# Kernel tuning notes

Hardware: AMD Instinct MI355X
Metric: run time of the kernel (lower is better)

Reference implementation:

```python
import jax, jax.numpy as jnp
import numpy as np

N = 50000      # nodes
E = 1200000    # edges
G = 256        # graphs in batch
H = 64         # hidden_dim
F_IN = 5       # input_dim
L = 3          # num deep GCN layers
EPS_BN = 1e-5
EPS_MSG = 1e-7

def setup_inputs() -> dict:
    key = jax.random.key(0)
    ks = jax.random.split(key, 12)
    r = lambda i, shp, s=0.1: jax.random.normal(ks[i], shp, jnp.float32) * s
    return {
        "x": jax.random.normal(ks[0], (N, F_IN), jnp.float32),
        "edge_index": jax.random.randint(ks[1], (2, E), 0, N),
        "batch_idx": jnp.sort(jax.random.randint(ks[2], (N,), 0, G)),
        "conv1_W": r(3, (F_IN, H)), "conv1_b": jnp.zeros((H,), jnp.float32),
        "bn1_g": jnp.ones((H,), jnp.float32), "bn1_b": jnp.zeros((H,), jnp.float32),
        "ln_g": jnp.ones((L, H), jnp.float32), "ln_b": jnp.zeros((L, H), jnp.float32),
        "prelu_a": jnp.full((L, H), 0.25, jnp.float32),
        "gen_t": jnp.ones((L,), jnp.float32),
        "mlp_W1": r(4, (L, H, 2 * H)), "mlp_b1": jnp.zeros((L, 2 * H), jnp.float32),
        "mlp_bn_g": jnp.ones((L, 2 * H), jnp.float32), "mlp_bn_b": jnp.zeros((L, 2 * H), jnp.float32),
        "mlp_W2": r(5, (L, 2 * H, H)), "mlp_b2": jnp.zeros((L, H), jnp.float32),
        "lin1_W": r(6, ((L + 1) * H * 2, 2 * H)), "lin1_b": jnp.zeros((2 * H,), jnp.float32),
        "lin2_W": r(7, (2 * H, H)), "lin2_b": jnp.zeros((H,), jnp.float32),
        "out_W": r(8, (H, 1)), "out_b": jnp.zeros((1,), jnp.float32),
    }

def _layernorm(x, g, b):
    mu = jnp.mean(x, axis=-1, keepdims=True)
    var = jnp.mean(jnp.square(x - mu), axis=-1, keepdims=True)
    return (x - mu) * jax.lax.rsqrt(var + EPS_BN) * g + b

def _prelu(x, a):
    return jnp.where(x >= 0, x, a * x)

def _bn_eval(x, g, b):
    # eval-mode BatchNorm with running_mean=0, running_var=1
    return x * (g / jnp.sqrt(1.0 + EPS_BN)) + b

def reference(x, edge_index, batch_idx, conv1_W, conv1_b, bn1_g, bn1_b,
              ln_g, ln_b, prelu_a, gen_t, mlp_W1, mlp_b1, mlp_bn_g, mlp_bn_b,
              mlp_W2, mlp_b2, lin1_W, lin1_b, lin2_W, lin2_b, out_W, out_b):
    n = x.shape[0]
    src, dst = edge_index[0], edge_index[1]

    # ---- GCNConv (with self loops, symmetric normalization) ----
    loops = jnp.arange(n)
    row = jnp.concatenate([src, loops])  # [E+N]
    col = jnp.concatenate([dst, loops])
    h = x @ conv1_W
    deg = jax.ops.segment_sum(jnp.ones_like(col, jnp.float32), col, num_segments=n)
    dinv = jnp.where(deg > 0, deg ** -0.5, 0.0)
    norm = dinv[row] * dinv[col]
    h = jax.ops.segment_sum(h[row] * norm[:, None], col, num_segments=n) + conv1_b
    h = _bn_eval(h, bn1_g, bn1_b)
    h = jax.nn.relu(h)

    xs = [h]
    # ---- DeepGCNLayer (res+) x L, GENConv with softmax aggregation ----
    for i in range(ln_g.shape[0]):
        u = _layernorm(h, ln_g[i], ln_b[i])
        u = _prelu(u, prelu_a[i])
        msg = jax.nn.relu(u[src]) + EPS_MSG            # [E, H]
        sc = msg * gen_t[i]
        m = jax.ops.segment_max(sc, dst, num_segments=n)
        e = jnp.exp(sc - m[dst])
        s = jax.ops.segment_sum(e, dst, num_segments=n)
        alpha = e / s[dst]                             # segment-wise softmax per channel
        agg = jax.ops.segment_sum(msg * alpha, dst, num_segments=n) + u  # root add
        z = agg @ mlp_W1[i] + mlp_b1[i]
        z = _bn_eval(z, mlp_bn_g[i], mlp_bn_b[i])
        z = jax.nn.relu(z)
        z = z @ mlp_W2[i] + mlp_b2[i]
        h = h + z                                      # res+
        xs.append(h)

    # ---- JumpingKnowledge cat + global mean/max pool ----
    xc = jnp.concatenate(xs, axis=1)                   # [N, 4H]
    cnt = jax.ops.segment_sum(jnp.ones((n,), jnp.float32), batch_idx, num_segments=G)
    xmean = jax.ops.segment_sum(xc, batch_idx, num_segments=G) / jnp.maximum(cnt, 1.0)[:, None]
    xmax = jax.ops.segment_max(xc, batch_idx, num_segments=G)
    xmax = jnp.where(jnp.isfinite(xmax), xmax, 0.0)
    p = jnp.concatenate([xmean, xmax], axis=1)         # [G, 8H]

    # ---- readout MLP (dropout off in eval) ----
    p = jax.nn.relu(p @ lin1_W + lin1_b)
    p = jax.nn.relu(p @ lin2_W + lin2_b)
    return p @ out_W + out_b
```

## Files before the change

kernel.cpp:

```cpp
#include <hip/hip_runtime.h>
#include <math.h>

#define NND 50000
#define NE  1200000
#define NG  256
#define H   64
#define H2  128
#define H4  256
#define H8  512
#define FIN 5
#define EPS_BN 1e-5f
#define EPS_MSG 1e-7f
#define NB 196
#define TILES 196
#define TCAP 7168
#define EPB 4096
#define NB1 293
#define MRG (NB + 14)
#define ELLC 72
#define MT 64

typedef _Float16 half8 __attribute__((ext_vector_type(8)));
typedef _Float16 half4 __attribute__((ext_vector_type(4)));
typedef float floatx4 __attribute__((ext_vector_type(4)));

__device__ __forceinline__ unsigned fmap_max(float f) {
    unsigned b = __float_as_uint(f);
    return (b & 0x80000000u) ? ~b : (b | 0x80000000u);
}


__global__ void __launch_bounds__(256)
k_setup(const int* __restrict__ batch, int* tilecur, int* __restrict__ gstart,
        const float* __restrict__ x, float* __restrict__ xp,
        const float* __restrict__ W1, const float* __restrict__ W2,
        _Float16* __restrict__ w1f, _Float16* __restrict__ w2f,
        const int* __restrict__ ei, unsigned* __restrict__ tilebuf) {
    __shared__ int cnt[TILES];
    __shared__ int base[TILES];
    int b = blockIdx.x, t = threadIdx.x;
    if (b >= MRG) {
        int bb = b - MRG;
        for (int i = t; i < TILES; i += 256) cnt[i] = 0;
        __syncthreads();
        int e0 = bb * EPB;
#pragma unroll
        for (int r = 0; r < EPB / 256; r++) {
            int e = e0 + r * 256 + t;
            if (e < NE) atomicAdd(&cnt[ei[NE + e] >> 8], 1);
        }
        __syncthreads();
        for (int i = t; i < TILES; i += 256) {
            base[i] = atomicAdd(&tilecur[i], cnt[i]);
            cnt[i] = 0;
        }
        __syncthreads();
#pragma unroll
        for (int r = 0; r < EPB / 256; r++) {
            int e = e0 + r * 256 + t;
            if (e < NE) {
                int s = ei[e], d = ei[NE + e];
                int tile = d >> 8;
                int pos = base[tile] + atomicAdd(&cnt[tile], 1);
                if (pos < TCAP)
                    tilebuf[(size_t)tile * TCAP + pos] = ((unsigned)s << 8) | (unsigned)(d & 255);
            }
        }
        return;
    }
    if (b < NB) {
        int n = b * 256 + t;
        if (n < NND) {
            float a0 = x[n * FIN + 0], a1 = x[n * FIN + 1], a2 = x[n * FIN + 2];
            float a3 = x[n * FIN + 3], a4 = x[n * FIN + 4];
            *(float4*)&xp[n * 8] = make_float4(a0, a1, a2, a3);
            *(float4*)&xp[n * 8 + 4] = make_float4(a4, 0.f, 0.f, 0.f);
        }
        return;
    }
    if (b == NB || b == NB + 1) {
        int g = (b - NB) * 256 + t;
        if (g > NG) return;
        int lo = 0, hi = NND;
        while (lo < hi) { int mid = (lo + hi) >> 1; if (batch[mid] < g) lo = mid + 1; else hi = mid; }
        gstart[g] = lo;
        return;
    }
    int tt = (b - NB - 2) * 256 + t;
    if (tt >= 3 * 16 * 64) return;
    int lane = tt & 63, fr = (tt >> 6) & 15, l = tt >> 10;
    {
        int jt = fr >> 1, kf = fr & 1;
        int j = jt * 16 + (lane & 15);
        int k0 = kf * 32 + (lane >> 4) * 8;
#pragma unroll
        for (int i = 0; i < 8; i++)
            w1f[(((size_t)l * 16 + jt * 2 + kf) * 64 + lane) * 8 + i] =
                (_Float16)W1[(size_t)l * H * H2 + (k0 + i) * H2 + j];
    }
    {
        int ct = fr >> 2, k2f = fr & 3;
        int c = ct * 16 + (lane & 15);
        int k0 = k2f * 32 + (lane >> 4) * 8;
#pragma unroll
        for (int i = 0; i < 8; i++)
            w2f[(((size_t)l * 16 + ct * 4 + k2f) * 64 + lane) * 8 + i] =
                (_Float16)W2[(size_t)l * H2 * H + (k0 + i) * H + c];
    }
}


__global__ void __launch_bounds__(256)
k_bin2(const int* __restrict__ tilecur, const unsigned* __restrict__ tilebuf,
       unsigned short* __restrict__ ell, int* __restrict__ deg, float* __restrict__ xp) {
    __shared__ unsigned short ell_l[256 * ELLC];
    __shared__ int cnt[256];
    int tile = blockIdx.x, t = threadIdx.x;
    cnt[t] = 0;
    __syncthreads();
    int n = min(tilecur[tile], TCAP);
    for (int i = t; i < n; i += 256) {
        unsigned v = __builtin_nontemporal_load(&tilebuf[(size_t)tile * TCAP + i]);
        int dl = v & 255u;
        int slot = atomicAdd(&cnt[dl], 1);
        if (slot < ELLC) ell_l[dl * ELLC + slot] = (unsigned short)(v >> 8);
    }
    __syncthreads();
    const unsigned* s32 = (const unsigned*)ell_l;
    unsigned* d32 = (unsigned*)(ell + (size_t)tile * 256 * ELLC);
    for (int i = t; i < 256 * ELLC / 2; i += 256) d32[i] = s32[i];
    int d = tile * 256 + t;
    if (d < NND) {
        deg[d] = min(cnt[t], ELLC);
        xp[(size_t)d * 8 + 5] = rsqrtf((float)cnt[t] + 1.0f);
    }
}


__global__ void k_gcn(const int* __restrict__ deg, const unsigned short* __restrict__ ell,
                      const float* __restrict__ xp,
                      const float* __restrict__ W,
                      const float* __restrict__ cb, const float* __restrict__ bg,
                      const float* __restrict__ bb,
                      const float* __restrict__ lg, const float* __restrict__ lb,
                      const float* __restrict__ pa,
                      _Float16* __restrict__ xcH, _Float16* __restrict__ u_h,
                      const int* __restrict__ batch,
                      float* __restrict__ psum, unsigned* __restrict__ pmax_u) {
    __shared__ float ps[4][64];
    __shared__ float pm[4][64];
    int tid = blockIdx.x * blockDim.x + threadIdx.x;
    int d = tid >> 4;
    int r = threadIdx.x & 15;
    if (d >= NND) return;
    int dg = deg[d];
    size_t base = (size_t)d * ELLC;
    float xw0 = 0.f, xw1 = 0.f, xw2 = 0.f, xw3 = 0.f, xw4 = 0.f;
    for (int i = r; i < dg; i += 16) {
        int s = (int)__builtin_nontemporal_load(&ell[base + i]);
        float4 a = *(const float4*)&xp[s * 8];
        float2 a45 = *(const float2*)&xp[s * 8 + 4];
        float dv = a45.y;
        xw0 += a.x * dv; xw1 += a.y * dv; xw2 += a.z * dv;
        xw3 += a.w * dv; xw4 += a45.x * dv;
    }
#pragma unroll
    for (int off = 1; off <= 8; off <<= 1) {
        xw0 += __shfl_xor(xw0, off, 64);
        xw1 += __shfl_xor(xw1, off, 64);
        xw2 += __shfl_xor(xw2, off, 64);
        xw3 += __shfl_xor(xw3, off, 64);
        xw4 += __shfl_xor(xw4, off, 64);
    }
    float4 xa = *(const float4*)&xp[d * 8];
    float2 xa45 = *(const float2*)&xp[d * 8 + 4];
    float dd = xa45.y;
    xw0 += dd * xa.x; xw1 += dd * xa.y; xw2 += dd * xa.z;
    xw3 += dd * xa.w; xw4 += dd * xa45.x;
    float bns = rsqrtf(1.f + EPS_BN);
    float x0[4];
    float sum = 0.f, sq = 0.f;
#pragma unroll
    for (int j = 0; j < 4; j++) {
        int c = 4 * r + j;
        float s_ = xw0 * W[c] + xw1 * W[H + c] + xw2 * W[2 * H + c]
                 + xw3 * W[3 * H + c] + xw4 * W[4 * H + c];
        float v = s_ * dd + cb[c];
        v = v * (bg[c] * bns) + bb[c];
        v = fmaxf(v, 0.f);
        x0[j] = v;
        sum += v; sq += v * v;
    }
    {
        half4 xh = {(_Float16)x0[0], (_Float16)x0[1], (_Float16)x0[2], (_Float16)x0[3]};
        *(half4*)&xcH[(size_t)d * H4 + 4 * r] = xh;
    }
#pragma unroll
    for (int off = 1; off <= 8; off <<= 1) {
        sum += __shfl_xor(sum, off, 64);
        sq  += __shfl_xor(sq,  off, 64);
    }
    float mu  = sum * (1.f / H);
    float var = sq * (1.f / H) - mu * mu;
    float rs = rsqrtf(var + EPS_BN);
    half4 yh;
#pragma unroll
    for (int j = 0; j < 4; j++) {
        int c = 4 * r + j;
        float y = (x0[j] - mu) * rs * lg[c] + lb[c];
        y = (y >= 0.f) ? y : pa[c] * y;
        yh[j] = (_Float16)y;
    }
    *(half4*)&u_h[(size_t)d * H + 4 * r] = yh;

    int first = blockIdx.x * 16;
    int gd = batch[d];
    int g_lo = batch[first], g_hi = batch[first + 15];
    int w = threadIdx.x >> 6;
    for (int g = g_lo; g <= g_hi; ++g) {
        bool m_ = (gd == g);
        float s0 = m_ ? x0[0] : 0.f, s1 = m_ ? x0[1] : 0.f;
        float s2 = m_ ? x0[2] : 0.f, s3 = m_ ? x0[3] : 0.f;
        float m0 = m_ ? x0[0] : -INFINITY, m1 = m_ ? x0[1] : -INFINITY;
        float m2 = m_ ? x0[2] : -INFINITY, m3 = m_ ? x0[3] : -INFINITY;
#pragma unroll
        for (int off = 16; off <= 32; off <<= 1) {
            s0 += __shfl_xor(s0, off, 64); s1 += __shfl_xor(s1, off, 64);
            s2 += __shfl_xor(s2, off, 64); s3 += __shfl_xor(s3, off, 64);
            m0 = fmaxf(m0, __shfl_xor(m0, off, 64)); m1 = fmaxf(m1, __shfl_xor(m1, off, 64));
            m2 = fmaxf(m2, __shfl_xor(m2, off, 64)); m3 = fmaxf(m3, __shfl_xor(m3, off, 64));
        }
        if ((threadIdx.x & 63) < 16) {
            ps[w][4 * r + 0] = s0; ps[w][4 * r + 1] = s1;
            ps[w][4 * r + 2] = s2; ps[w][4 * r + 3] = s3;
            pm[w][4 * r + 0] = m0; pm[w][4 * r + 1] = m1;
            pm[w][4 * r + 2] = m2; pm[w][4 * r + 3] = m3;
        }
        __syncthreads();
        if (threadIdx.x < 64) {
            float S = (ps[0][threadIdx.x] + ps[1][threadIdx.x]) +
                      (ps[2][threadIdx.x] + ps[3][threadIdx.x]);
            float M = fmaxf(fmaxf(pm[0][threadIdx.x], pm[1][threadIdx.x]),
                            fmaxf(pm[2][threadIdx.x], pm[3][threadIdx.x]));
            atomicAdd(&psum[(size_t)g * H4 + threadIdx.x], S);
            atomicMax(&pmax_u[(size_t)g * H4 + threadIdx.x], fmap_max(M));
        }
        __syncthreads();
    }
}


__global__ void k_gen(const int* __restrict__ deg, const unsigned short* __restrict__ ell,
                      const _Float16* __restrict__ u_h,
                      const float* __restrict__ tptr, int li, _Float16* __restrict__ ua_h) {
    int d = (blockIdx.x * blockDim.x + threadIdx.x) >> 6;
    int lane = threadIdx.x & 63;
    if (d >= NND) return;
    int q = lane & 15, eg = lane >> 4;
    float t = tptr[li];
    int dg = deg[d];
    size_t base = (size_t)d * ELLC;
    half4 us = *(const half4*)&u_h[(size_t)d * H + 4 * q];
    float4 s4 = {0.f, 0.f, 0.f, 0.f}, n4 = {0.f, 0.f, 0.f, 0.f};
    for (int i0 = 0; i0 < dg; i0 += 64) {
        int idx = i0 + lane;
        int csrv = (idx < dg) ? (int)__builtin_nontemporal_load(&ell[base + idx]) : 0;
        int chunk = min(64, dg - i0);
        for (int j = 0; j < chunk; j += 32) {
            half4 uv[8]; bool ok[8];
#pragma unroll
            for (int b2 = 0; b2 < 8; b2++) {
                int e_rel = j + 4 * b2 + eg;
                int s = __shfl(csrv, e_rel, 64);
                ok[b2] = (e_rel < chunk);
                uv[b2] = (half4){0, 0, 0, 0};
                if (ok[b2]) uv[b2] = *(const half4*)&u_h[(size_t)s * H + 4 * q];
            }
#pragma unroll
            for (int b2 = 0; b2 < 8; b2++) {
                if (ok[b2]) {
                    float m0 = fmaxf((float)uv[b2][0], 0.f) + EPS_MSG;
                    float m1 = fmaxf((float)uv[b2][1], 0.f) + EPS_MSG;
                    float m2 = fmaxf((float)uv[b2][2], 0.f) + EPS_MSG;
                    float m3 = fmaxf((float)uv[b2][3], 0.f) + EPS_MSG;
                    float e0 = __expf(m0 * t - 8.f);
                    float e1 = __expf(m1 * t - 8.f);
                    float e2 = __expf(m2 * t - 8.f);
                    float e3 = __expf(m3 * t - 8.f);
                    s4.x += e0; s4.y += e1; s4.z += e2; s4.w += e3;
                    n4.x += m0 * e0; n4.y += m1 * e1; n4.z += m2 * e2; n4.w += m3 * e3;
                }
            }
        }
    }
#pragma unroll
    for (int off = 16; off <= 32; off <<= 1) {
        s4.x += __shfl_xor(s4.x, off, 64); s4.y += __shfl_xor(s4.y, off, 64);
        s4.z += __shfl_xor(s4.z, off, 64); s4.w += __shfl_xor(s4.w, off, 64);
        n4.x += __shfl_xor(n4.x, off, 64); n4.y += __shfl_xor(n4.y, off, 64);
        n4.z += __shfl_xor(n4.z, off, 64); n4.w += __shfl_xor(n4.w, off, 64);
    }
    if (eg == 0) {
        float o0 = (float)us[0] + ((s4.x > 0.f) ? n4.x / s4.x : 0.f);
        float o1 = (float)us[1] + ((s4.y > 0.f) ? n4.y / s4.y : 0.f);
        float o2 = (float)us[2] + ((s4.z > 0.f) ? n4.z / s4.z : 0.f);
        float o3 = (float)us[3] + ((s4.w > 0.f) ? n4.w / s4.w : 0.f);
        half4 oh = {(_Float16)o0, (_Float16)o1, (_Float16)o2, (_Float16)o3};
        *(half4*)&ua_h[(size_t)d * H + 4 * q] = oh;
    }
}


__global__ void __launch_bounds__(256)
k_mlp(const _Float16* __restrict__ ua_h,
      const _Float16* __restrict__ w1f, const _Float16* __restrict__ w2f,
      const float* __restrict__ b1,
      const float* __restrict__ bng, const float* __restrict__ bnb,
      const float* __restrict__ b2,
      _Float16* __restrict__ xcH, int slice,
      const float* __restrict__ lg, const float* __restrict__ lb,
      const float* __restrict__ pa, _Float16* __restrict__ u_h, int do_ln,
      const int* __restrict__ batch,
      float* __restrict__ psum, unsigned* __restrict__ pmax_u) {
    __shared__ _Float16 a2[4][4][64][8];
    __shared__ float pls[4][64];
    __shared__ float plm[4][64];
    int t = threadIdx.x;
    int w = t >> 6, l = t & 63;
    int nb = blockIdx.x * MT;
    int c_in = l & 15, quad = l >> 4;
    bool wvalid = (nb + 16 * w) < NND;

    half8 af0 = {0,0,0,0,0,0,0,0}, af1 = af0;
    {
        int node = nb + 16 * w + c_in;
        if (node < NND) {
            af0 = *(const half8*)&ua_h[(size_t)node * H + quad * 8];
            af1 = *(const half8*)&ua_h[(size_t)node * H + 32 + quad * 8];
        }
    }

    floatx4 acc[8];
#pragma unroll
    for (int jt = 0; jt < 8; jt++) acc[jt] = (floatx4){0.f, 0.f, 0.f, 0.f};
#pragma unroll
    for (int jt = 0; jt < 8; jt++) {
        half8 bf0 = *(const half8*)&w1f[((size_t)(jt * 2 + 0) * 64 + l) * 8];
        half8 bf1 = *(const half8*)&w1f[((size_t)(jt * 2 + 1) * 64 + l) * 8];
        acc[jt] = __builtin_amdgcn_mfma_f32_16x16x32_f16(af0, bf0, acc[jt], 0, 0, 0);
        acc[jt] = __builtin_amdgcn_mfma_f32_16x16x32_f16(af1, bf1, acc[jt], 0, 0, 0);
    }

    {
        float bns = rsqrtf(1.f + EPS_BN);
#pragma unroll
        for (int jt = 0; jt < 8; jt++) {
            int j = jt * 16 + c_in;
            float b1v = b1[j], bsv = bng[j] * bns, bbv = bnb[j];
            int kf2 = jt >> 1;
            int lp = 16 * ((2 * jt + (c_in >> 3)) & 3);
            int ii = c_in & 7;
#pragma unroll
            for (int reg = 0; reg < 4; reg++) {
                float z = fmaxf((acc[jt][reg] + b1v) * bsv + bbv, 0.f);
                a2[w][kf2][quad * 4 + reg + lp][ii] = (_Float16)z;
            }
        }
    }

    floatx4 acc2[4];
#pragma unroll
    for (int ct = 0; ct < 4; ct++) acc2[ct] = (floatx4){0.f, 0.f, 0.f, 0.f};
    half8 a2f[4];
#pragma unroll
    for (int k2f = 0; k2f < 4; k2f++) a2f[k2f] = *(half8*)&a2[w][k2f][l][0];
#pragma unroll
    for (int ct = 0; ct < 4; ct++) {
#pragma unroll
        for (int k2f = 0; k2f < 4; k2f++) {
            half8 bfr = *(const half8*)&w2f[((size_t)(ct * 4 + k2f) * 64 + l) * 8];
            acc2[ct] = __builtin_amdgcn_mfma_f32_16x16x32_f16(a2f[k2f], bfr, acc2[ct], 0, 0, 0);
        }
    }

    float vv[4][4];
#pragma unroll
    for (int ct = 0; ct < 4; ct++) {
        int c = ct * 16 + c_in;
        float b2v = b2[c];
#pragma unroll
        for (int reg = 0; reg < 4; reg++) {
            int node = nb + 16 * w + quad * 4 + reg;
            float v = 0.f;
            if (wvalid) {
                v = (float)xcH[(size_t)node * H4 + slice * H + c] + acc2[ct][reg] + b2v;
                xcH[(size_t)node * H4 + (slice + 1) * H + c] = (_Float16)v;
            }
            vv[ct][reg] = v;
        }
    }
    if (do_ln) {
#pragma unroll
        for (int reg = 0; reg < 4; reg++) {
            float s = (vv[0][reg] + vv[1][reg]) + (vv[2][reg] + vv[3][reg]);
            float q = (vv[0][reg] * vv[0][reg] + vv[1][reg] * vv[1][reg]) +
                      (vv[2][reg] * vv[2][reg] + vv[3][reg] * vv[3][reg]);
#pragma unroll
            for (int off = 1; off <= 8; off <<= 1) {
                s += __shfl_xor(s, off, 64);
                q += __shfl_xor(q, off, 64);
            }
            float mu = s * (1.f / H);
            float var = q * (1.f / H) - mu * mu;
            float rs = rsqrtf(var + EPS_BN);
            int node = nb + 16 * w + quad * 4 + reg;
#pragma unroll
            for (int ct = 0; ct < 4; ct++) {
                int c = ct * 16 + c_in;
                float y = (vv[ct][reg] - mu) * rs * lg[c] + lb[c];
                y = (y >= 0.f) ? y : pa[c] * y;
                if (wvalid) u_h[(size_t)node * H + c] = (_Float16)y;
            }
        }
    }

    int gd_r[4];
#pragma unroll
    for (int reg = 0; reg < 4; reg++) {
        int node = nb + 16 * w + quad * 4 + reg;
        gd_r[reg] = (node < NND) ? batch[node] : -1;
    }
    int g_lo = batch[nb];
    int g_hi = batch[min(nb + 63, NND - 1)];
    int chbase = (slice + 1) * H;
    for (int g = g_lo; g <= g_hi; ++g) {
        float sc[4], mc[4];
#pragma unroll
        for (int ct = 0; ct < 4; ct++) {
            float s_ = 0.f, m_ = -INFINITY;
#pragma unroll
            for (int reg = 0; reg < 4; reg++) {
                if (gd_r[reg] == g) { s_ += vv[ct][reg]; m_ = fmaxf(m_, vv[ct][reg]); }
            }
            sc[ct] = s_; mc[ct] = m_;
        }
#pragma unroll
        for (int off = 16; off <= 32; off <<= 1) {
#pragma unroll
            for (int ct = 0; ct < 4; ct++) {
                sc[ct] += __shfl_xor(sc[ct], off, 64);
                mc[ct] = fmaxf(mc[ct], __shfl_xor(mc[ct], off, 64));
            }
        }
        if (l < 16) {
#pragma unroll
            for (int ct = 0; ct < 4; ct++) {
                pls[w][ct * 16 + l] = sc[ct];
                plm[w][ct * 16 + l] = mc[ct];
            }
        }
        __syncthreads();
        if (t < 64) {
            float S = (pls[0][t] + pls[1][t]) + (pls[2][t] + pls[3][t]);
            float M = fmaxf(fmaxf(plm[0][t], plm[1][t]), fmaxf(plm[2][t], plm[3][t]));
            atomicAdd(&psum[(size_t)g * H4 + chbase + t], S);
            atomicMax(&pmax_u[(size_t)g * H4 + chbase + t], fmap_max(M));
        }
        __syncthreads();
    }
}


__global__ void __launch_bounds__(256)
k_readout(const float* __restrict__ psum, const unsigned* __restrict__ pmax_u,
          const int* __restrict__ gstart,
          const float* __restrict__ W1, const float* __restrict__ b1,
          const float* __restrict__ W2, const float* __restrict__ b2,
          const float* __restrict__ Wo, const float* __restrict__ bo,
          float* __restrict__ out) {
    __shared__ float p0_l[H8];
    __shared__ float p1part[2][H2];
    __shared__ float p1_l[H2];
    __shared__ float p2part[4][H];
    __shared__ float p2_l[H];
    int g = blockIdx.x;
    int t = threadIdx.x;

    {
        int cnt = gstart[g + 1] - gstart[g];
        float s = psum[(size_t)g * H4 + t];
        unsigned u = pmax_u[(size_t)g * H4 + t];
        float m = (u & 0x80000000u) ? __uint_as_float(u & 0x7FFFFFFFu) : __uint_as_float(~u);
        p0_l[t] = s / fmaxf((float)cnt, 1.f);
        p0_l[H4 + t] = (cnt > 0) ? m : 0.f;
    }
    __syncthreads();

    {
        int j = t & 127, h = t >> 7;
        float acc = 0.f;
        int k0 = h * 256;
        for (int k = 0; k < 256; k++) acc += p0_l[k0 + k] * W1[(k0 + k) * H2 + j];
        p1part[h][j] = acc;
    }
    __syncthreads();
    if (t < H2) p1_l[t] = fmaxf(p1part[0][t] + p1part[1][t] + b1[t], 0.f);
    __syncthreads();

    {
        int c = t & 63, h = t >> 6;
        float acc = 0.f;
        int k0 = h * 32;
        for (int k = 0; k < 32; k++) acc += p1_l[k0 + k] * W2[(k0 + k) * H + c];
        p2part[h][c] = acc;
    }
    __syncthreads();
    if (t < H) p2_l[t] = fmaxf(((p2part[0][t] + p2part[1][t]) + (p2part[2][t] + p2part[3][t])) + b2[t], 0.f);
    __syncthreads();

    if (t < 64) {
        float v = p2_l[t] * Wo[t];
#pragma unroll
        for (int off = 32; off >= 1; off >>= 1) v += __shfl_xor(v, off, 64);
        if (t == 0) out[g] = v + bo[0];
    }
}

extern "C" void kernel_launch(void* const* d_in, const int* in_sizes, int n_in,
                              void* d_out, int out_size, void* d_ws, size_t ws_size,
                              hipStream_t stream) {
    const float* x       = (const float*)d_in[0];
    const int*   ei      = (const int*)d_in[1];
    const int*   batch   = (const int*)d_in[2];
    const float* conv1_W = (const float*)d_in[3];
    const float* conv1_b = (const float*)d_in[4];
    const float* bn1_g   = (const float*)d_in[5];
    const float* bn1_b   = (const float*)d_in[6];
    const float* ln_g    = (const float*)d_in[7];
    const float* ln_b    = (const float*)d_in[8];
    const float* prelu_a = (const float*)d_in[9];
    const float* gen_t   = (const float*)d_in[10];
    const float* mlp_W1  = (const float*)d_in[11];
    const float* mlp_b1  = (const float*)d_in[12];
    const float* mlp_bng = (const float*)d_in[13];
    const float* mlp_bnb = (const float*)d_in[14];
    const float* mlp_W2  = (const float*)d_in[15];
    const float* mlp_b2  = (const float*)d_in[16];
    const float* lin1_W  = (const float*)d_in[17];
    const float* lin1_b  = (const float*)d_in[18];
    const float* lin2_W  = (const float*)d_in[19];
    const float* lin2_b  = (const float*)d_in[20];
    const float* out_W   = (const float*)d_in[21];
    const float* out_b   = (const float*)d_in[22];
    float* out = (float*)d_out;

    float* ws   = (float*)d_ws;
    _Float16* xcH = (_Float16*)ws;
    float* xp   = (float*)(xcH + (size_t)NND * H4);
    int* deg    = (int*)(xp + (size_t)NND * 8);
    int* gstart = deg + NND;
    int* tilecur = gstart + NG + 1;
    unsigned* tilebuf = (unsigned*)(tilecur + TILES);
    unsigned short* ell = (unsigned short*)(tilebuf + (size_t)TILES * TCAP);
    uintptr_t wb = (uintptr_t)(ell + (size_t)TILES * 256 * ELLC);
    wb = (wb + 15) & ~(uintptr_t)15;
    _Float16* w1f = (_Float16*)wb;
    _Float16* w2f = w1f + 3 * 8192;
    _Float16* u_h  = w2f + 3 * 8192;
    _Float16* ua_h = u_h + (size_t)NND * H;
    uintptr_t pb = (uintptr_t)(ua_h + (size_t)NND * H);
    pb = (pb + 15) & ~(uintptr_t)15;
    float* psum = (float*)pb;
    unsigned* pmax_u = (unsigned*)(psum + (size_t)NG * H4);

    const int B = 256;
    const int gGCN = (NND * 16 + B - 1) / B;
    const int gNH  = (NND * H) / B;
    const int gMLP = (NND + MT - 1) / MT;

    hipMemsetAsync(tilecur, 0, TILES * sizeof(int), stream);
    hipMemsetAsync(psum, 0, (size_t)NG * H4 * (sizeof(float) + sizeof(unsigned)), stream);
    k_setup<<<MRG + NB1, B, 0, stream>>>(batch, tilecur, gstart, x, xp,
                                         mlp_W1, mlp_W2, w1f, w2f, ei, tilebuf);
    k_bin2<<<TILES, B, 0, stream>>>(tilecur, tilebuf, ell, deg, xp);

    k_gcn<<<gGCN, B, 0, stream>>>(deg, ell, xp, conv1_W, conv1_b, bn1_g, bn1_b,
                                  ln_g, ln_b, prelu_a, xcH, u_h,
                                  batch, psum, pmax_u);

    for (int i = 0; i < 3; i++) {
        k_gen<<<gNH, B, 0, stream>>>(deg, ell, u_h, gen_t, i, ua_h);
        int do_ln = (i < 2) ? 1 : 0;
        k_mlp<<<gMLP, B, 0, stream>>>(ua_h,
                                      w1f + (size_t)i * 8192, w2f + (size_t)i * 8192,
                                      mlp_b1 + i * H2,
                                      mlp_bng + i * H2, mlp_bnb + i * H2,
                                      mlp_b2 + i * H,
                                      xcH, i,
                                      ln_g + (i + 1) * H, ln_b + (i + 1) * H,
                                      prelu_a + (i + 1) * H, u_h, do_ln,
                                      batch, psum, pmax_u);
    }

    k_readout<<<NG, B, 0, stream>>>(psum, pmax_u, gstart,
                                    lin1_W, lin1_b, lin2_W, lin2_b, out_W, out_b, out);
}
```

Before: 332.8 us.

## Precompute per-node softmax exp terms in producer kernels instead of per edge

The GENConv softmax numerator and weighted message terms (exp(m*t) and m*exp(m*t)) are now computed once per source node in k_gcn and k_mlp and stored as interleaved fp16 in a new buffer. k_gen then only gathers and sums these precomputed pairs per edge instead of evaluating exp for every edge. This removes per-edge transcendental work but doubles the bytes gathered per edge and adds fp16 rounding and overflow risk on the exp values.

```diff
diff --git a/kernel.cpp b/kernel.cpp
--- a/kernel.cpp
+++ b/kernel.cpp
@@ -22,6 +22,7 @@
 
 typedef _Float16 half8 __attribute__((ext_vector_type(8)));
 typedef _Float16 half4 __attribute__((ext_vector_type(4)));
+typedef _Float16 half2 __attribute__((ext_vector_type(2)));
 typedef float floatx4 __attribute__((ext_vector_type(4)));
 
 __device__ __forceinline__ unsigned fmap_max(float f) {
@@ -146,7 +147,8 @@
                       const float* __restrict__ pa,
                       _Float16* __restrict__ xcH, _Float16* __restrict__ u_h,
                       const int* __restrict__ batch,
-                      float* __restrict__ psum, unsigned* __restrict__ pmax_u) {
+                      float* __restrict__ psum, unsigned* __restrict__ pmax_u,
+                      const float* __restrict__ gent, _Float16* __restrict__ emf) {
     __shared__ float ps[4][64];
     __shared__ float pm[4][64];
     int tid = blockIdx.x * blockDim.x + threadIdx.x;
@@ -203,15 +205,22 @@
     float mu  = sum * (1.f / H);
     float var = sq * (1.f / H) - mu * mu;
     float rs = rsqrtf(var + EPS_BN);
+    float t0 = gent[0];
     half4 yh;
+    half8 emh;
 #pragma unroll
     for (int j = 0; j < 4; j++) {
         int c = 4 * r + j;
         float y = (x0[j] - mu) * rs * lg[c] + lb[c];
         y = (y >= 0.f) ? y : pa[c] * y;
         yh[j] = (_Float16)y;
+        float m_ = fmaxf(y, 0.f) + EPS_MSG;
+        float ex = __expf(m_ * t0 - 8.f);
+        emh[2 * j]     = (_Float16)ex;
+        emh[2 * j + 1] = (_Float16)(m_ * ex);
     }
     *(half4*)&u_h[(size_t)d * H + 4 * r] = yh;
+    *(half8*)&emf[(size_t)d * 128 + 8 * r] = emh;
 
     int first = blockIdx.x * 16;
     int gd = batch[d];
@@ -251,13 +260,12 @@
 
 
 __global__ void k_gen(const int* __restrict__ deg, const unsigned short* __restrict__ ell,
-                      const _Float16* __restrict__ u_h,
-                      const float* __restrict__ tptr, int li, _Float16* __restrict__ ua_h) {
+                      const _Float16* __restrict__ u_h, const _Float16* __restrict__ emf,
+                      _Float16* __restrict__ ua_h) {
     int d = (blockIdx.x * blockDim.x + threadIdx.x) >> 6;
     int lane = threadIdx.x & 63;
     if (d >= NND) return;
     int q = lane & 15, eg = lane >> 4;
-    float t = tptr[li];
     int dg = deg[d];
     size_t base = (size_t)d * ELLC;
     half4 us = *(const half4*)&u_h[(size_t)d * H + 4 * q];
@@ -267,29 +275,20 @@
         int csrv = (idx < dg) ? (int)__builtin_nontemporal_load(&ell[base + idx]) : 0;
         int chunk = min(64, dg - i0);
         for (int j = 0; j < chunk; j += 32) {
-            half4 uv[8]; bool ok[8];
+            half8 uv[8];
 #pragma unroll
             for (int b2 = 0; b2 < 8; b2++) {
                 int e_rel = j + 4 * b2 + eg;
                 int s = __shfl(csrv, e_rel, 64);
-                ok[b2] = (e_rel < chunk);
-                uv[b2] = (half4){0, 0, 0, 0};
-                if (ok[b2]) uv[b2] = *(const half4*)&u_h[(size_t)s * H + 4 * q];
+                uv[b2] = (half8){0, 0, 0, 0, 0, 0, 0, 0};
+                if (e_rel < chunk) uv[b2] = *(const half8*)&emf[(size_t)s * 128 + 8 * q];
             }
 #pragma unroll
             for (int b2 = 0; b2 < 8; b2++) {
-                if (ok[b2]) {
-                    float m0 = fmaxf((float)uv[b2][0], 0.f) + EPS_MSG;
-                    float m1 = fmaxf((float)uv[b2][1], 0.f) + EPS_MSG;
-                    float m2 = fmaxf((float)uv[b2][2], 0.f) + EPS_MSG;
-                    float m3 = fmaxf((float)uv[b2][3], 0.f) + EPS_MSG;
-                    float e0 = __expf(m0 * t - 8.f);
-                    float e1 = __expf(m1 * t - 8.f);
-                    float e2 = __expf(m2 * t - 8.f);
-                    float e3 = __expf(m3 * t - 8.f);
-                    s4.x += e0; s4.y += e1; s4.z += e2; s4.w += e3;
-                    n4.x += m0 * e0; n4.y += m1 * e1; n4.z += m2 * e2; n4.w += m3 * e3;
-                }
+                s4.x += (float)uv[b2][0]; n4.x += (float)uv[b2][1];
+                s4.y += (float)uv[b2][2]; n4.y += (float)uv[b2][3];
+                s4.z += (float)uv[b2][4]; n4.z += (float)uv[b2][5];
+                s4.w += (float)uv[b2][6]; n4.w += (float)uv[b2][7];
             }
         }
     }
@@ -321,7 +320,8 @@
       const float* __restrict__ lg, const float* __restrict__ lb,
       const float* __restrict__ pa, _Float16* __restrict__ u_h, int do_ln,
       const int* __restrict__ batch,
-      float* __restrict__ psum, unsigned* __restrict__ pmax_u) {
+      float* __restrict__ psum, unsigned* __restrict__ pmax_u,
+      const float* __restrict__ gent, _Float16* __restrict__ emf) {
     __shared__ _Float16 a2[4][4][64][8];
     __shared__ float pls[4][64];
     __shared__ float plm[4][64];
@@ -400,6 +400,7 @@
         }
     }
     if (do_ln) {
+        float t1 = gent[slice + 1];
 #pragma unroll
         for (int reg = 0; reg < 4; reg++) {
             float s = (vv[0][reg] + vv[1][reg]) + (vv[2][reg] + vv[3][reg]);
@@ -419,7 +420,13 @@
                 int c = ct * 16 + c_in;
                 float y = (vv[ct][reg] - mu) * rs * lg[c] + lb[c];
                 y = (y >= 0.f) ? y : pa[c] * y;
-                if (wvalid) u_h[(size_t)node * H + c] = (_Float16)y;
+                float m_ = fmaxf(y, 0.f) + EPS_MSG;
+                float ex = __expf(m_ * t1 - 8.f);
+                if (wvalid) {
+                    u_h[(size_t)node * H + c] = (_Float16)y;
+                    half2 p = {(_Float16)ex, (_Float16)(m_ * ex)};
+                    *(half2*)&emf[(size_t)node * 128 + 2 * c] = p;
+                }
             }
         }
     }
@@ -568,7 +575,8 @@
     _Float16* w2f = w1f + 3 * 8192;
     _Float16* u_h  = w2f + 3 * 8192;
     _Float16* ua_h = u_h + (size_t)NND * H;
-    uintptr_t pb = (uintptr_t)(ua_h + (size_t)NND * H);
+    _Float16* emf  = ua_h + (size_t)NND * H;
+    uintptr_t pb = (uintptr_t)(emf + (size_t)NND * 128);
     pb = (pb + 15) & ~(uintptr_t)15;
     float* psum = (float*)pb;
     unsigned* pmax_u = (unsigned*)(psum + (size_t)NG * H4);
@@ -586,10 +594,10 @@
 
     k_gcn<<<gGCN, B, 0, stream>>>(deg, ell, xp, conv1_W, conv1_b, bn1_g, bn1_b,
                                   ln_g, ln_b, prelu_a, xcH, u_h,
-                                  batch, psum, pmax_u);
+                                  batch, psum, pmax_u, gen_t, emf);
 
     for (int i = 0; i < 3; i++) {
-        k_gen<<<gNH, B, 0, stream>>>(deg, ell, u_h, gen_t, i, ua_h);
+        k_gen<<<gNH, B, 0, stream>>>(deg, ell, u_h, emf, ua_h);
         int do_ln = (i < 2) ? 1 : 0;
         k_mlp<<<gMLP, B, 0, stream>>>(ua_h,
                                       w1f + (size_t)i * 8192, w2f + (size_t)i * 8192,
@@ -599,7 +607,7 @@
                                       xcH, i,
                                       ln_g + (i + 1) * H, ln_b + (i + 1) * H,
                                       prelu_a + (i + 1) * H, u_h, do_ln,
-                                      batch, psum, pmax_u);
+                                      batch, psum, pmax_u, gen_t, emf);
     }
 
     k_readout<<<NG, B, 0, stream>>>(psum, pmax_u, gstart,
```

Result: slower. 388.9 us (+16.8%).
